# Kernel optimization log

Hardware: AMD Instinct MI355X
Metric: run time of the kernel (lower is better)

The kernel has to match this reference:

```python
import jax, jax.numpy as jnp
import numpy as np

NEG = -1e12


def setup_inputs() -> dict:
    key = jax.random.key(0)
    ks = jax.random.split(key, 10)
    B, C, Q, D = 16, 384, 64, 2048
    return {
        "c": jax.random.normal(ks[0], (B, C, D), dtype=jnp.float32),
        "q": jax.random.normal(ks[1], (B, Q, D), dtype=jnp.float32),
        "c_len": jax.random.randint(ks[2], (B,), 1, C + 1),
        "q_len": jax.random.randint(ks[3], (B,), 1, Q + 1),
        "w_c": jax.random.normal(ks[4], (D,), dtype=jnp.float32) * 0.02,
        "b_c": jnp.zeros((), dtype=jnp.float32),
        "w_q": jax.random.normal(ks[5], (D,), dtype=jnp.float32) * 0.02,
        "b_q": jnp.zeros((), dtype=jnp.float32),
        "w_cq": jax.random.normal(ks[6], (D,), dtype=jnp.float32) * 0.02,
        "b_cq": jnp.zeros((), dtype=jnp.float32),
        "W_out": jax.random.normal(ks[7], (4 * D, 2), dtype=jnp.float32) * 0.02,
        "b_out": jnp.zeros((2,), dtype=jnp.float32),
    }


def reference(c, q, c_len, q_len, w_c, b_c, w_q, b_q, w_cq, b_cq, W_out, b_out):
    B, C, D = c.shape
    Q = q.shape[1]
    # trilinear similarity: s[b,r,i] = w_c.c_r + w_q.q_i + w_cq.(c_r*q_i) + biases
    cq = jnp.einsum('bcd,bqd,d->bcq', c, q, w_cq) + b_cq          # [B,C,Q]
    s = (c @ w_c + b_c)[:, :, None] + (q @ w_q + b_q)[:, None, :] + cq
    rows = jnp.arange(C)[None, :, None]
    cols = jnp.arange(Q)[None, None, :]
    # faithful to the triple loop: cols >= q_len OR (rows >= c_len AND col < Q-1)
    masked = (cols >= q_len[:, None, None]) | (
        (rows >= c_len[:, None, None]) & (cols < Q - 1))
    s = s + jnp.where(masked, jnp.float32(NEG), jnp.float32(0.0))
    a = jax.nn.softmax(s, axis=2)                                  # [B,C,Q]
    c2q = jnp.einsum('bcq,bqd->bcd', a, q)                         # [B,C,D]
    b_att = jax.nn.softmax(jnp.max(s, axis=2), axis=1)             # [B,C]
    q2c = jnp.einsum('bc,bcd->bd', b_att, c)[:, None, :]           # [B,1,D]
    x = jnp.concatenate(
        [c, c2q, c * c2q, c * jnp.broadcast_to(q2c, c.shape)], axis=-1)
    out = x @ W_out + b_out                                        # [B,C,2]
    # final masking: out[i][c_len[i]:-1] = NEG (last row untouched)
    row_mask = (jnp.arange(C)[None, :] >= c_len[:, None]) & (
        jnp.arange(C)[None, :] < C - 1)
    out = jnp.where(row_mask[..., None], jnp.float32(NEG), out)
    return out[..., 0], out[..., 1]
```

## Files before the change

### kernel.cpp

```cpp
#include <hip/hip_runtime.h>

#define NEGV -1.0e12f
constexpr int B = 16, C = 384, Q = 64, D = 2048;
constexpr int PITCH = 40;
constexpr int IST = 8320;
constexpr int NIMG = 64;
constexpr int NT = 96;
constexpr int KC = 4;
constexpr int SP = 208;

typedef __attribute__((ext_vector_type(8))) short s16x8;
typedef __attribute__((ext_vector_type(4))) float f32x4;

__device__ __forceinline__ unsigned pkbf(float lo, float hi) {
  unsigned ulo = __builtin_bit_cast(unsigned, lo);
  unsigned uhi = __builtin_bit_cast(unsigned, hi);
  return (uhi & 0xFFFF0000u) | (ulo >> 16);
}
__device__ __forceinline__ float bflo(unsigned u) {
  return __builtin_bit_cast(float, u << 16);
}
__device__ __forceinline__ float bfhi(unsigned u) {
  return __builtin_bit_cast(float, u & 0xFFFF0000u);
}
__device__ __forceinline__ float bfs(unsigned short u) {
  return __builtin_bit_cast(float, ((unsigned)u) << 16);
}

#define GLD_LDS(gsrc, ldst)                                              \
  __builtin_amdgcn_global_load_lds(                                      \
      (const __attribute__((address_space(1))) unsigned*)(gsrc),         \
      (__attribute__((address_space(3))) unsigned*)(ldst), 16, 0, 0)

__global__ __launch_bounds__(256) void k_pq(
    const float* __restrict__ q, const float* __restrict__ w_cq,
    const float* __restrict__ w_c, const float* __restrict__ w_q,
    const float* __restrict__ W_out, unsigned short* __restrict__ bpk,
    float* __restrict__ qstats) {
  const int t = threadIdx.x;
  if (blockIdx.x < 512) {
    const int s = blockIdx.x & 31, b = blockIdx.x >> 5;
    const int k0 = s * 64;
    unsigned short* base = bpk + (size_t)b * NIMG * IST;
#pragma unroll
    for (int i = 0; i < 4; ++i) {
      int idx = t + 256 * i;
      int qi = idx >> 4, kc = (idx & 15) * 4;
      unsigned short* img = base + (size_t)(s * 2 + (kc >> 5)) * IST;
      const int ko = kc & 31;
      float4 qv = *(const float4*)(q + ((size_t)b * Q + qi) * D + k0 + kc);
      float4 wq = *(const float4*)(w_cq + k0 + kc);
      const float* wp = W_out + (size_t)(2 * D + k0 + kc) * 2;
      float4 wa = *(const float4*)(wp);
      float4 wb = *(const float4*)(wp + 4);
      uint2 u;
      u.x = pkbf(qv.x * wq.x, qv.y * wq.y);
      u.y = pkbf(qv.z * wq.z, qv.w * wq.w);
      *(uint2*)(img + qi * PITCH + ko) = u;
      u.x = pkbf(qv.x * wa.x, qv.y * wa.z);
      u.y = pkbf(qv.z * wb.x, qv.w * wb.z);
      *(uint2*)(img + (64 + qi) * PITCH + ko) = u;
      u.x = pkbf(qv.x * wa.y, qv.y * wa.w);
      u.y = pkbf(qv.z * wb.y, qv.w * wb.w);
      *(uint2*)(img + (128 + qi) * PITCH + ko) = u;
    }
    if (t < 48) {
      int r = t >> 4, kc = (t & 15) * 4;
      unsigned short* img = base + (size_t)(s * 2 + (kc >> 5)) * IST;
      const int ko = kc & 31;
      uint2 u;
      if (r == 0) {
        float4 w = *(const float4*)(w_c + k0 + kc);
        u.x = pkbf(w.x, w.y);
        u.y = pkbf(w.z, w.w);
      } else {
        const float* wp = W_out + (size_t)(k0 + kc) * 2 + (r - 1);
        u.x = pkbf(wp[0], wp[2]);
        u.y = pkbf(wp[4], wp[6]);
      }
      *(uint2*)(img + (192 + r) * PITCH + ko) = u;
    }
  } else {
    int bi = blockIdx.x - 512;
    const float* qrow = q + (size_t)bi * D;
    float a0 = 0.f, a1 = 0.f, a2 = 0.f;
    for (int d = t * 4; d < D; d += 256 * 4) {
      float4 qv = *(const float4*)(qrow + d);
      float4 wq = *(const float4*)(w_q + d);
      const float* wp = W_out + (size_t)(D + d) * 2;
      float4 wa = *(const float4*)(wp);
      float4 wb = *(const float4*)(wp + 4);
      a0 += qv.x * wq.x + qv.y * wq.y + qv.z * wq.z + qv.w * wq.w;
      a1 += qv.x * wa.x + qv.y * wa.z + qv.z * wb.x + qv.w * wb.z;
      a2 += qv.x * wa.y + qv.y * wa.w + qv.z * wb.y + qv.w * wb.w;
    }
    for (int m = 1; m < 64; m <<= 1) {
      a0 += __shfl_xor(a0, m, 64);
      a1 += __shfl_xor(a1, m, 64);
      a2 += __shfl_xor(a2, m, 64);
    }
    __shared__ float red[3][4];
    int w = t >> 6, lane = t & 63;
    if (lane == 0) { red[0][w] = a0; red[1][w] = a1; red[2][w] = a2; }
    __syncthreads();
    if (t == 0) {
      qstats[bi * 3 + 0] = red[0][0] + red[0][1] + red[0][2] + red[0][3];
      qstats[bi * 3 + 1] = red[1][0] + red[1][1] + red[1][2] + red[1][3];
      qstats[bi * 3 + 2] = red[2][0] + red[2][1] + red[2][2] + red[2][3];
    }
  }
}

__global__ __launch_bounds__(512, 1) void k_score(
    const unsigned short* __restrict__ bpk, const float* __restrict__ c,
    unsigned short* __restrict__ S3pb, unsigned short* __restrict__ cbf) {
  const int t = threadIdx.x;
  const int lane = t & 63, wv = t >> 6;
  const int bid = blockIdx.x;
  const int b = bid & 15, kcb = (bid >> 4) & 3, n0 = (bid >> 6) * NT;
  const int lr = lane & 15, lg = lane >> 4;
  const int mg = wv >> 1, ng = wv & 1;

  __shared__ unsigned short sBp[3][IST];
  __shared__ unsigned short sCp[3][NT * PITCH];

  const unsigned short* gB = bpk + ((size_t)b * NIMG + kcb * 16) * IST;
  const float* cbase = c + ((size_t)b * C + n0) * D + kcb * 512;
  unsigned short* cbf_base = cbf + ((size_t)b * C + n0) * D + kcb * 512;

  f32x4 acc[4][3];
#pragma unroll
  for (int f = 0; f < 4; ++f)
#pragma unroll
    for (int g = 0; g < 3; ++g) acc[f][g] = f32x4{0.f, 0.f, 0.f, 0.f};

  auto stageB = [&](int buf, int s) {
    const char* src = (const char*)gB + (size_t)s * (IST * 2);
    char* dst = (char*)&sBp[buf][0];
    GLD_LDS(src + t * 16, dst + t * 16);
    GLD_LDS(src + 8192 + t * 16, dst + 8192 + t * 16);
    if (t < 16) GLD_LDS(src + 16384 + t * 16, dst + 16384 + t * 16);
  };
  auto loadC = [&](float4* r, int s) {
    const float* base = cbase + s * 32;
    if (wv < 4) {
      int g0 = wv * 128 + lane;
      r[0] = *(const float4*)(base + (size_t)(g0 >> 3) * D + (g0 & 7) * 4);
      int g1 = g0 + 64;
      r[1] = *(const float4*)(base + (size_t)(g1 >> 3) * D + (g1 & 7) * 4);
    } else {
      int g0 = 512 + (wv - 4) * 64 + lane;
      r[0] = *(const float4*)(base + (size_t)(g0 >> 3) * D + (g0 & 7) * 4);
    }
  };
  auto writeC = [&](int buf, const float4* r, int s) {
    unsigned short* cb = cbf_base + s * 32;
    if (wv < 4) {
      int g0 = wv * 128 + lane;
      uint2 u0 = {pkbf(r[0].x, r[0].y), pkbf(r[0].z, r[0].w)};
      *(uint2*)&sCp[buf][(g0 >> 3) * PITCH + (g0 & 7) * 4] = u0;
      *(uint2*)(cb + (size_t)(g0 >> 3) * D + (g0 & 7) * 4) = u0;
      int g1 = g0 + 64;
      uint2 u1 = {pkbf(r[1].x, r[1].y), pkbf(r[1].z, r[1].w)};
      *(uint2*)&sCp[buf][(g1 >> 3) * PITCH + (g1 & 7) * 4] = u1;
      *(uint2*)(cb + (size_t)(g1 >> 3) * D + (g1 & 7) * 4) = u1;
    } else {
      int g0 = 512 + (wv - 4) * 64 + lane;
      uint2 u0 = {pkbf(r[0].x, r[0].y), pkbf(r[0].z, r[0].w)};
      *(uint2*)&sCp[buf][(g0 >> 3) * PITCH + (g0 & 7) * 4] = u0;
      *(uint2*)(cb + (size_t)(g0 >> 3) * D + (g0 & 7) * 4) = u0;
    }
  };
  auto compute = [&](int buf) {
    s16x8 af[4], bf[3];
#pragma unroll
    for (int f = 0; f < 4; ++f)
      af[f] = *(const s16x8*)&sBp[buf][(mg * 64 + f * 16 + lr) * PITCH +
                                       lg * 8];
#pragma unroll
    for (int g = 0; g < 3; ++g)
      bf[g] = *(const s16x8*)&sCp[buf][((ng * 3 + g) * 16 + lr) * PITCH +
                                       lg * 8];
#pragma unroll
    for (int f = 0; f < 4; ++f)
#pragma unroll
      for (int g = 0; g < 3; ++g)
        acc[f][g] =
            __builtin_amdgcn_mfma_f32_16x16x32_bf16(af[f], bf[g], acc[f][g],
                                                    0, 0, 0);
  };

  auto vmwait2 = [&]() {
    if (wv == 0)
      asm volatile("s_waitcnt vmcnt(14)" ::: "memory");
    else if (wv < 4)
      asm volatile("s_waitcnt vmcnt(12)" ::: "memory");
    else
      asm volatile("s_waitcnt vmcnt(8)" ::: "memory");
  };
  auto vmwait1 = [&]() {
    if (wv == 0)
      asm volatile("s_waitcnt vmcnt(7)" ::: "memory");
    else if (wv < 4)
      asm volatile("s_waitcnt vmcnt(6)" ::: "memory");
    else
      asm volatile("s_waitcnt vmcnt(4)" ::: "memory");
  };

  float4 rc[3][2];
  stageB(0, 0);
  loadC(rc[0], 0);
  stageB(1, 1);
  loadC(rc[1], 1);
#pragma unroll
  for (int s = 0; s < 16; ++s) {
    const int cur = s % 3;
    if (s + 2 < 16) {
      stageB((s + 2) % 3, s + 2);
      loadC(rc[(s + 2) % 3], s + 2);
      vmwait2();
    } else if (s + 1 < 16) {
      vmwait1();
    } else {
      asm volatile("s_waitcnt vmcnt(0)" ::: "memory");
    }
    writeC(cur, rc[cur], s);
    asm volatile("s_waitcnt lgkmcnt(0)" ::: "memory");
    __builtin_amdgcn_sched_barrier(0);
    __builtin_amdgcn_s_barrier();
    compute(cur);
    __builtin_amdgcn_s_barrier();
  }

  const size_t rowbase = ((size_t)kcb * B + b) * C;
#pragma unroll
  for (int f = 0; f < 4; ++f) {
    int mf = mg * 4 + f;
    if (mf < 13) {
#pragma unroll
      for (int g = 0; g < 3; ++g) {
        int n = n0 + (ng * 3 + g) * 16 + lr;
        uint2 pk;
        pk.x = pkbf(acc[f][g][0], acc[f][g][1]);
        pk.y = pkbf(acc[f][g][2], acc[f][g][3]);
        *(uint2*)(S3pb + (rowbase + n) * SP + mf * 16 + lg * 4) = pk;
      }
    }
  }
}

__global__ __launch_bounds__(256) void k_soft(
    const unsigned short* __restrict__ S3pb, const float* __restrict__ qstats,
    const int* __restrict__ c_len, const int* __restrict__ q_len,
    const float* __restrict__ b_c, const float* __restrict__ b_q,
    const float* __restrict__ b_cq, float* __restrict__ mrow,
    float* __restrict__ out12) {
  const int t = threadIdx.x, lane = t & 63;
  const int rg = blockIdx.x * 4 + (t >> 6);
  const int b = rg / C, r = rg % C;
  float s_cq = 0.f, sc = 0.f, w10 = 0.f, w11 = 0.f, t30 = 0.f, t31 = 0.f;
#pragma unroll
  for (int p = 0; p < KC; ++p) {
    const unsigned short* Sr = S3pb + ((size_t)p * B * C + rg) * SP;
    s_cq += bfs(Sr[lane]);
    sc += bfs(Sr[192]);
    w10 += bfs(Sr[193]);
    w11 += bfs(Sr[194]);
    t30 += bfs(Sr[64 + lane]);
    t31 += bfs(Sr[128 + lane]);
  }
  const float qs0 = qstats[((b << 6) + lane) * 3 + 0];
  const float qs1 = qstats[((b << 6) + lane) * 3 + 1];
  const float qs2 = qstats[((b << 6) + lane) * 3 + 2];
  float s = s_cq + sc + qs0 + b_c[0] + b_q[0] + b_cq[0];
  const int cl = c_len[b], ql = q_len[b];
  bool masked = (lane >= ql) || ((r >= cl) && (lane < Q - 1));
  if (masked) s += NEGV;
  float mx = s;
  for (int m = 1; m < 64; m <<= 1) mx = fmaxf(mx, __shfl_xor(mx, m, 64));
  float e = __expf(s - mx);
  float den = e;
  for (int m = 1; m < 64; m <<= 1) den += __shfl_xor(den, m, 64);
  float a = e / den;
  float v0 = a * (qs1 + t30);
  float v1 = a * (qs2 + t31);
  for (int m = 1; m < 64; m <<= 1) {
    v0 += __shfl_xor(v0, m, 64);
    v1 += __shfl_xor(v1, m, 64);
  }
  if (lane == 0) {
    mrow[rg] = mx;
    out12[rg * 2 + 0] = w10 + v0;
    out12[rg * 2 + 1] = w11 + v1;
  }
}

__global__ __launch_bounds__(512) void k_q2cu(
    const unsigned short* __restrict__ cbf, const float* __restrict__ mrow,
    const float* __restrict__ W_out, float* __restrict__ uvec) {
  const int ch = blockIdx.x, b = blockIdx.y;
  const int t = threadIdx.x, lane = t & 63, wv = t >> 6;
  __shared__ float batt[C];
  __shared__ float rmx[8], rsm[8];
  __shared__ float redq0[8][64], redq1[8][64];

  float m = (t < C) ? mrow[b * C + t] : -3.0e38f;
  float mx = m;
  for (int o = 1; o < 64; o <<= 1) mx = fmaxf(mx, __shfl_xor(mx, o, 64));
  if (lane == 0) rmx[wv] = mx;
  __syncthreads();
  mx = rmx[0];
#pragma unroll
  for (int i = 1; i < 8; ++i) mx = fmaxf(mx, rmx[i]);
  float e = (t < C) ? __expf(m - mx) : 0.f;
  float sm = e;
  for (int o = 1; o < 64; o <<= 1) sm += __shfl_xor(sm, o, 64);
  if (lane == 0) rsm[wv] = sm;
  __syncthreads();
  sm = rsm[0] + rsm[1] + rsm[2] + rsm[3] + rsm[4] + rsm[5] + rsm[6] + rsm[7];
  if (t < C) batt[t] = e / sm;
  __syncthreads();

  const int d0 = ch * 128 + lane * 2;
  const unsigned short* p = cbf + ((size_t)b * C + wv * 8) * D + d0;
  float A0[8] = {0.f, 0.f, 0.f, 0.f, 0.f, 0.f, 0.f, 0.f};
  float A1[8] = {0.f, 0.f, 0.f, 0.f, 0.f, 0.f, 0.f, 0.f};
#pragma unroll
  for (int r0 = 0; r0 < 384; r0 += 64) {
    const unsigned short* pr = p + (size_t)r0 * D;
    const float* bt = &batt[r0 + wv * 8];
#pragma unroll
    for (int j = 0; j < 8; ++j) {
      unsigned cc = *(const unsigned*)(pr + (size_t)j * D);
      A0[j] += bt[j] * bflo(cc);
      A1[j] += bt[j] * bfhi(cc);
    }
  }
  float s0 = ((A0[0] + A0[1]) + (A0[2] + A0[3])) +
             ((A0[4] + A0[5]) + (A0[6] + A0[7]));
  float s1 = ((A1[0] + A1[1]) + (A1[2] + A1[3])) +
             ((A1[4] + A1[5]) + (A1[6] + A1[7]));
  redq0[wv][lane] = s0;
  redq1[wv][lane] = s1;
  __syncthreads();
  if (t < 64) {
    float q0 = 0.f, q1 = 0.f;
#pragma unroll
    for (int w = 0; w < 8; ++w) {
      q0 += redq0[w][t];
      q1 += redq1[w][t];
    }
    int dd = ch * 128 + t * 2;
    float4 w4 = *(const float4*)(W_out + (size_t)(3 * D + dd) * 2);
    float4 u = {q0 * w4.x, q0 * w4.y, q1 * w4.z, q1 * w4.w};
    *(float4*)(uvec + ((size_t)b * D + dd) * 2) = u;
  }
}

__global__ __launch_bounds__(512) void k_out(
    const unsigned short* __restrict__ cbf, const float* __restrict__ uvec,
    const float* __restrict__ out12, const float* __restrict__ b_out,
    const int* __restrict__ c_len, float* __restrict__ outp) {
  const int b = blockIdx.y, r0 = blockIdx.x * 8;
  const int t = threadIdx.x, lane = t & 63, wv = t >> 6;
  __shared__ float u_sh[2 * D];

  {
    const float* src = uvec + (size_t)b * D * 2 + t * 8;
    float4 v0 = *(const float4*)(src);
    float4 v1 = *(const float4*)(src + 4);
    *(float4*)&u_sh[t * 8] = v0;
    *(float4*)&u_sh[t * 8 + 4] = v1;
  }
  __syncthreads();

  const int r = r0 + wv;
  const unsigned short* crow = cbf + ((size_t)b * C + r) * D;
  float o0 = 0.f, o1 = 0.f;
#pragma unroll
  for (int it = 0; it < 16; ++it) {
    int d0 = it * 128 + lane * 2;
    unsigned cc = *(const unsigned*)(crow + d0);
    float c0 = bflo(cc), c1 = bfhi(cc);
    float4 u = *(const float4*)&u_sh[d0 * 2];
    o0 += c0 * u.x + c1 * u.z;
    o1 += c0 * u.y + c1 * u.w;
  }
  for (int o = 1; o < 64; o <<= 1) {
    o0 += __shfl_xor(o0, o, 64);
    o1 += __shfl_xor(o1, o, 64);
  }
  if (lane == 0) {
    const int idx = b * C + r;
    o0 += out12[idx * 2 + 0] + b_out[0];
    o1 += out12[idx * 2 + 1] + b_out[1];
    if (r >= c_len[b] && r < C - 1) { o0 = NEGV; o1 = NEGV; }
    outp[idx] = o0;
    outp[B * C + idx] = o1;
  }
}

extern "C" void kernel_launch(void* const* d_in, const int* in_sizes, int n_in,
                              void* d_out, int out_size, void* d_ws,
                              size_t ws_size, hipStream_t stream) {
  const float* c = (const float*)d_in[0];
  const float* q = (const float*)d_in[1];
  const int* c_len = (const int*)d_in[2];
  const int* q_len = (const int*)d_in[3];
  const float* w_c = (const float*)d_in[4];
  const float* b_c = (const float*)d_in[5];
  const float* w_q = (const float*)d_in[6];
  const float* b_q = (const float*)d_in[7];
  const float* w_cq = (const float*)d_in[8];
  const float* b_cq = (const float*)d_in[9];
  const float* W_out = (const float*)d_in[10];
  const float* b_out = (const float*)d_in[11];
  float* outp = (float*)d_out;

  unsigned short* bpk = (unsigned short*)d_ws;
  const size_t bpk_bytes = (size_t)B * NIMG * IST * 2;
  unsigned short* S3pb = (unsigned short*)((char*)d_ws + bpk_bytes);
  const size_t s3_elems = (size_t)KC * B * C * SP;
  float* ws = (float*)(S3pb + s3_elems);
  float* qstats = ws;
  float* mrow = ws + 3072;
  float* out12 = ws + 3072 + 6144;
  float* uvec = ws + 3072 + 6144 + 12288;
  unsigned short* cbf = (unsigned short*)(uvec + 65536);

  hipLaunchKernelGGL(k_pq, dim3(512 + B * Q), dim3(256), 0, stream, q, w_cq,
                     w_c, w_q, W_out, bpk, qstats);
  hipLaunchKernelGGL(k_score, dim3(4 * KC * B), dim3(512), 0, stream, bpk, c,
                     S3pb, cbf);
  hipLaunchKernelGGL(k_soft, dim3(B * C / 4), dim3(256), 0, stream, S3pb,
                     qstats, c_len, q_len, b_c, b_q, b_cq, mrow, out12);
  hipLaunchKernelGGL(k_q2cu, dim3(16, B), dim3(512), 0, stream, cbf, mrow,
                     W_out, uvec);
  hipLaunchKernelGGL(k_out, dim3(C / 8, B), dim3(512), 0, stream, cbf, uvec,
                     out12, b_out, c_len, outp);
}
```

Baseline: 47.91 us.

## Double K-step size in score kernel with double-buffered 64-wide stages

The score GEMM's main loop changes from 16 stages of K=32 with triple buffering to 8 stages of K=64 with double buffering. Each stage loads two B images and a 64-column C tile, and the hand-tuned vmcnt waits are recomputed for the new load counts. The aim is to halve barrier and synchronisation overhead per unit of work and issue larger loads. In exchange the prefetch distance shrinks to one stage and LDS use per buffer grows. The vmcnt wait values are fragile and could break correctness if the counts are wrong.

```diff
diff --git a/kernel.cpp b/kernel.cpp
--- a/kernel.cpp
+++ b/kernel.cpp
@@ -8,6 +8,7 @@
 constexpr int NT = 96;
 constexpr int KC = 4;
 constexpr int SP = 208;
+constexpr int CP = 72;
 
 typedef __attribute__((ext_vector_type(8))) short s16x8;
 typedef __attribute__((ext_vector_type(4))) float f32x4;
@@ -121,8 +122,8 @@
   const int lr = lane & 15, lg = lane >> 4;
   const int mg = wv >> 1, ng = wv & 1;
 
-  __shared__ unsigned short sBp[3][IST];
-  __shared__ unsigned short sCp[3][NT * PITCH];
+  __shared__ unsigned short sBp[2][2 * IST];
+  __shared__ unsigned short sCp[2][NT * CP];
 
   const unsigned short* gB = bpk + ((size_t)b * NIMG + kcb * 16) * IST;
   const float* cbase = c + ((size_t)b * C + n0) * D + kcb * 512;
@@ -135,94 +136,83 @@
     for (int g = 0; g < 3; ++g) acc[f][g] = f32x4{0.f, 0.f, 0.f, 0.f};
 
   auto stageB = [&](int buf, int s) {
-    const char* src = (const char*)gB + (size_t)s * (IST * 2);
+    const char* src = (const char*)gB + (size_t)s * 33280;
     char* dst = (char*)&sBp[buf][0];
     GLD_LDS(src + t * 16, dst + t * 16);
     GLD_LDS(src + 8192 + t * 16, dst + 8192 + t * 16);
-    if (t < 16) GLD_LDS(src + 16384 + t * 16, dst + 16384 + t * 16);
+    GLD_LDS(src + 16384 + t * 16, dst + 16384 + t * 16);
+    GLD_LDS(src + 24576 + t * 16, dst + 24576 + t * 16);
+    if (t < 32) GLD_LDS(src + 32768 + t * 16, dst + 32768 + t * 16);
   };
   auto loadC = [&](float4* r, int s) {
-    const float* base = cbase + s * 32;
-    if (wv < 4) {
-      int g0 = wv * 128 + lane;
-      r[0] = *(const float4*)(base + (size_t)(g0 >> 3) * D + (g0 & 7) * 4);
-      int g1 = g0 + 64;
-      r[1] = *(const float4*)(base + (size_t)(g1 >> 3) * D + (g1 & 7) * 4);
-    } else {
-      int g0 = 512 + (wv - 4) * 64 + lane;
-      r[0] = *(const float4*)(base + (size_t)(g0 >> 3) * D + (g0 & 7) * 4);
+    const float* base = cbase + s * 64;
+#pragma unroll
+    for (int i = 0; i < 3; ++i) {
+      int g = t + 512 * i;
+      r[i] = *(const float4*)(base + (size_t)(g >> 4) * D + (g & 15) * 4);
     }
   };
   auto writeC = [&](int buf, const float4* r, int s) {
-    unsigned short* cb = cbf_base + s * 32;
-    if (wv < 4) {
-      int g0 = wv * 128 + lane;
-      uint2 u0 = {pkbf(r[0].x, r[0].y), pkbf(r[0].z, r[0].w)};
-      *(uint2*)&sCp[buf][(g0 >> 3) * PITCH + (g0 & 7) * 4] = u0;
-      *(uint2*)(cb + (size_t)(g0 >> 3) * D + (g0 & 7) * 4) = u0;
-      int g1 = g0 + 64;
-      uint2 u1 = {pkbf(r[1].x, r[1].y), pkbf(r[1].z, r[1].w)};
-      *(uint2*)&sCp[buf][(g1 >> 3) * PITCH + (g1 & 7) * 4] = u1;
-      *(uint2*)(cb + (size_t)(g1 >> 3) * D + (g1 & 7) * 4) = u1;
-    } else {
-      int g0 = 512 + (wv - 4) * 64 + lane;
-      uint2 u0 = {pkbf(r[0].x, r[0].y), pkbf(r[0].z, r[0].w)};
-      *(uint2*)&sCp[buf][(g0 >> 3) * PITCH + (g0 & 7) * 4] = u0;
-      *(uint2*)(cb + (size_t)(g0 >> 3) * D + (g0 & 7) * 4) = u0;
+    unsigned short* cb = cbf_base + s * 64;
+#pragma unroll
+    for (int i = 0; i < 3; ++i) {
+      int g = t + 512 * i;
+      uint2 u = {pkbf(r[i].x, r[i].y), pkbf(r[i].z, r[i].w)};
+      *(uint2*)&sCp[buf][(g >> 4) * CP + (g & 15) * 4] = u;
+      *(uint2*)(cb + (size_t)(g >> 4) * D + (g & 15) * 4) = u;
     }
   };
   auto compute = [&](int buf) {
-    s16x8 af[4], bf[3];
-#pragma unroll
-    for (int f = 0; f < 4; ++f)
-      af[f] = *(const s16x8*)&sBp[buf][(mg * 64 + f * 16 + lr) * PITCH +
-                                       lg * 8];
-#pragma unroll
-    for (int g = 0; g < 3; ++g)
-      bf[g] = *(const s16x8*)&sCp[buf][((ng * 3 + g) * 16 + lr) * PITCH +
-                                       lg * 8];
-#pragma unroll
-    for (int f = 0; f < 4; ++f)
+#pragma unroll
+    for (int h = 0; h < 2; ++h) {
+      s16x8 af[4], bf[3];
+#pragma unroll
+      for (int f = 0; f < 4; ++f)
+        af[f] = *(const s16x8*)&sBp[buf][h * IST +
+                                         (mg * 64 + f * 16 + lr) * PITCH +
+                                         lg * 8];
 #pragma unroll
       for (int g = 0; g < 3; ++g)
-        acc[f][g] =
-            __builtin_amdgcn_mfma_f32_16x16x32_bf16(af[f], bf[g], acc[f][g],
-                                                    0, 0, 0);
-  };
-
-  auto vmwait2 = [&]() {
+        bf[g] = *(const s16x8*)&sCp[buf][((ng * 3 + g) * 16 + lr) * CP +
+                                         h * 32 + lg * 8];
+#pragma unroll
+      for (int f = 0; f < 4; ++f)
+#pragma unroll
+        for (int g = 0; g < 3; ++g)
+          acc[f][g] =
+              __builtin_amdgcn_mfma_f32_16x16x32_bf16(af[f], bf[g], acc[f][g],
+                                                      0, 0, 0);
+    }
+  };
+
+  auto vmwait_first = [&]() {
     if (wv == 0)
-      asm volatile("s_waitcnt vmcnt(14)" ::: "memory");
-    else if (wv < 4)
-      asm volatile("s_waitcnt vmcnt(12)" ::: "memory");
+      asm volatile("s_waitcnt vmcnt(8)" ::: "memory");
     else
-      asm volatile("s_waitcnt vmcnt(8)" ::: "memory");
-  };
-  auto vmwait1 = [&]() {
+      asm volatile("s_waitcnt vmcnt(7)" ::: "memory");
+  };
+  auto vmwait_mid = [&]() {
     if (wv == 0)
-      asm volatile("s_waitcnt vmcnt(7)" ::: "memory");
-    else if (wv < 4)
-      asm volatile("s_waitcnt vmcnt(6)" ::: "memory");
+      asm volatile("s_waitcnt vmcnt(11)" ::: "memory");
     else
-      asm volatile("s_waitcnt vmcnt(4)" ::: "memory");
-  };
-
-  float4 rc[3][2];
+      asm volatile("s_waitcnt vmcnt(10)" ::: "memory");
+  };
+
+  float4 rc[2][3];
   stageB(0, 0);
   loadC(rc[0], 0);
-  stageB(1, 1);
-  loadC(rc[1], 1);
-#pragma unroll
-  for (int s = 0; s < 16; ++s) {
-    const int cur = s % 3;
-    if (s + 2 < 16) {
-      stageB((s + 2) % 3, s + 2);
-      loadC(rc[(s + 2) % 3], s + 2);
-      vmwait2();
-    } else if (s + 1 < 16) {
-      vmwait1();
+#pragma unroll
+  for (int s = 0; s < 8; ++s) {
+    const int cur = s & 1;
+    if (s + 1 < 8) {
+      stageB(cur ^ 1, s + 1);
+      loadC(rc[cur ^ 1], s + 1);
+      if (s == 0)
+        vmwait_first();
+      else
+        vmwait_mid();
     } else {
-      asm volatile("s_waitcnt vmcnt(0)" ::: "memory");
+      asm volatile("s_waitcnt vmcnt(3)" ::: "memory");
     }
     writeC(cur, rc[cur], s);
     asm volatile("s_waitcnt lgkmcnt(0)" ::: "memory");
```

Result: no change. 48.46 us (+1.2%).
